# Optimization experiments

Hardware: AMD Instinct MI355X
Metric: run time of the kernel (lower is better)

Reference implementation:

```python
import jax, jax.numpy as jnp
import numpy as np

HEADS = 8
DIM_HEAD = 64
SCALE = DIM_HEAD ** -0.5


def setup_inputs() -> dict:
    key = jax.random.key(0)
    k1, k2, k3 = jax.random.split(key, 3)
    b, n, dim = 2, 4096, 512
    inner = HEADS * DIM_HEAD
    x = jax.random.normal(k1, (b, n, dim), dtype=jnp.float32)
    w_qkv = jax.random.normal(k2, (dim, 3 * inner), dtype=jnp.float32) * (dim ** -0.5)
    w_out = jax.random.normal(k3, (inner, dim), dtype=jnp.float32) * (inner ** -0.5)
    b_out = jnp.zeros((dim,), dtype=jnp.float32)
    return {"x": x, "w_qkv": w_qkv, "w_out": w_out, "b_out": b_out}


def reference(x, w_qkv, w_out, b_out):
    b, n, dim = x.shape
    qkv = x @ w_qkv  # [b, n, 3*inner]
    q, k, v = jnp.split(qkv, 3, axis=-1)
    # b n (h d) -> b h n d
    split_heads = lambda t: t.reshape(b, n, HEADS, DIM_HEAD).transpose(0, 2, 1, 3)
    q, k, v = split_heads(q), split_heads(k), split_heads(v)
    dots = jnp.einsum('bhid,bhjd->bhij', q, k) * SCALE  # [b, h, n, n]
    attn = jax.nn.log_softmax(dots, axis=-1)  # NOTE: log-softmax, not softmax
    out = jnp.einsum('bhij,bhjd->bhid', attn, v)  # [b, h, n, d]
    out = out.transpose(0, 2, 1, 3).reshape(b, n, HEADS * DIM_HEAD)
    return out @ w_out + b_out + x
```

## Files before the change

kernel.cpp:

```cpp
#include <hip/hip_runtime.h>
#include <stdint.h>

#define NSEQ   4096
#define BATCH  2
#define NHEAD  8
#define DHEAD  64
#define DIM    512
#define NQKV   1536
#define MROWS  (BATCH*NSEQ)
#define NBH    (BATCH*NHEAD)

typedef float  f32x4 __attribute__((ext_vector_type(4)));
typedef short  s16x8 __attribute__((ext_vector_type(8)));

__device__ __forceinline__ unsigned short f2b(float f){
  unsigned int u = __float_as_uint(f);
  u += 0x7FFFu + ((u >> 16) & 1u);
  return (unsigned short)(u >> 16);
}
__device__ __forceinline__ float b2f(unsigned short h){
  return __uint_as_float(((unsigned int)h) << 16);
}
__device__ __forceinline__ void gld_lds16(const void* g, void* l){
  __builtin_amdgcn_global_load_lds((const __attribute__((address_space(1))) unsigned int*)g,
                                   (__attribute__((address_space(3))) unsigned int*)l, 16, 0, 0);
}

__global__ void k_cvt(const float* __restrict__ in, unsigned short* __restrict__ out, int n4){
  int i = blockIdx.x*blockDim.x + threadIdx.x;
  if (i < n4){
    float4 v = ((const float4*)in)[i];
    ushort4 o;
    o.x = f2b(v.x); o.y = f2b(v.y); o.z = f2b(v.z); o.w = f2b(v.w);
    ((ushort4*)out)[i] = o;
  }
}

__global__ void k_transpose(const float* __restrict__ in, unsigned short* __restrict__ out, int R, int C){
  __shared__ float t[32][33];
  const int cb = blockIdx.x*32, rb = blockIdx.y*32;
  const int tx = threadIdx.x & 31, ty = threadIdx.x >> 5;
  #pragma unroll
  for (int s = 0; s < 32; s += 8) t[ty+s][tx] = in[(size_t)(rb+ty+s)*C + cb + tx];
  __syncthreads();
  #pragma unroll
  for (int s = 0; s < 32; s += 8) out[(size_t)(cb+ty+s)*R + rb + tx] = f2b(t[tx][ty+s]);
}

__global__ __launch_bounds__(256) void k_qkv_gemm(
    const unsigned short* __restrict__ A,
    const unsigned short* __restrict__ Bt,
    unsigned short* __restrict__ qbuf, unsigned short* __restrict__ kbuf,
    unsigned short* __restrict__ vbuf){
  __shared__ __align__(16) unsigned short at[128*32];
  __shared__ __align__(16) unsigned short bt[128*32];
  const int n0 = blockIdx.x*128, m0 = blockIdx.y*128;
  const int tid = threadIdx.x, w = tid>>6, lane = tid&63;
  const int wr = (w>>1)*64, wc = (w&1)*64;
  f32x4 acc[4][4] = {};
  for (int ks = 0; ks < 16; ++ks){
    const int k0 = ks*32;
    #pragma unroll
    for (int i = 0; i < 2; ++i){
      const int slot = w*2 + i;
      const int r = slot*16 + (lane>>2);
      const int ch = (lane&3) ^ (r&3);
      gld_lds16(A  + (size_t)(m0+r)*DIM + k0 + ch*8, (char*)at + slot*1024);
      gld_lds16(Bt + (size_t)(n0+r)*DIM + k0 + ch*8, (char*)bt + slot*1024);
    }
    __syncthreads();
    s16x8 af[4], bfr[4];
    #pragma unroll
    for (int f = 0; f < 4; ++f){
      const int rr = wr + f*16 + (lane&15);
      af[f]  = *(const s16x8*)((const char*)at + rr*64 + ((((lane>>4)) ^ (rr&3))<<4));
      const int cc = wc + f*16 + (lane&15);
      bfr[f] = *(const s16x8*)((const char*)bt + cc*64 + ((((lane>>4)) ^ (cc&3))<<4));
    }
    #pragma unroll
    for (int fr = 0; fr < 4; ++fr)
      #pragma unroll
      for (int fc = 0; fc < 4; ++fc)
        acc[fr][fc] = __builtin_amdgcn_mfma_f32_16x16x32_bf16(af[fr], bfr[fc], acc[fr][fc], 0,0,0);
    __syncthreads();
  }
  const float QS = 0.18033688011112042f;
  #pragma unroll
  for (int fr = 0; fr < 4; ++fr){
    #pragma unroll
    for (int fc = 0; fc < 4; ++fc){
      const int col = n0 + wc + fc*16 + (lane&15);
      const int which = col >> 9;
      const int h = (col & 511) >> 6;
      const int d = col & 63;
      unsigned short* dst = (which==0) ? qbuf : ((which==1) ? kbuf : vbuf);
      #pragma unroll
      for (int r = 0; r < 4; ++r){
        const int row = m0 + wr + fr*16 + (lane>>4)*4 + r;
        const int b = row >> 12, n = row & 4095;
        float v = acc[fr][fc][r];
        if (which == 0) v *= QS;
        dst[(size_t)((b*NHEAD + h)*NSEQ + n)*DHEAD + d] = f2b(v);
      }
    }
  }
}

__global__ __launch_bounds__(256) void k_tpart(
    const unsigned short* __restrict__ kbuf, const unsigned short* __restrict__ vbuf,
    float* __restrict__ tpart, float* __restrict__ vsp){
  __shared__ __align__(16) unsigned short kt[64*64];
  __shared__ __align__(16) unsigned short vt[64*64];
  const int bh = blockIdx.y, jc = blockIdx.x;
  const unsigned short* K = kbuf + (size_t)bh*NSEQ*DHEAD;
  const unsigned short* V = vbuf + (size_t)bh*NSEQ*DHEAD;
  const int tid = threadIdx.x;
  const int d1 = (tid>>4)<<2, d2 = (tid&15)<<2;
  const int j0 = jc*64;
  #pragma unroll
  for (int c = 0; c < 2; ++c){
    const int q = tid + 256*c;
    const int row = q>>3, ch = q&7;
    *(float4*)((char*)kt + row*128 + ch*16) = *(const float4*)((const char*)K + (size_t)(j0+row)*128 + ch*16);
    *(float4*)((char*)vt + row*128 + ch*16) = *(const float4*)((const char*)V + (size_t)(j0+row)*128 + ch*16);
  }
  __syncthreads();
  float accT[4][4] = {{0.f}};
  float accV[4] = {0.f,0.f,0.f,0.f};
  for (int jj = 0; jj < 64; ++jj){
    const ushort4 k4 = *(const ushort4*)(kt + jj*64 + d1);
    const ushort4 v4 = *(const ushort4*)(vt + jj*64 + d2);
    float kf[4] = {b2f(k4.x), b2f(k4.y), b2f(k4.z), b2f(k4.w)};
    float vf[4] = {b2f(v4.x), b2f(v4.y), b2f(v4.z), b2f(v4.w)};
    #pragma unroll
    for (int a = 0; a < 4; ++a)
      #pragma unroll
      for (int b = 0; b < 4; ++b) accT[a][b] += kf[a]*vf[b];
    #pragma unroll
    for (int b = 0; b < 4; ++b) accV[b] += vf[b];
  }
  float* tp = tpart + ((size_t)bh*64 + jc)*4096;
  #pragma unroll
  for (int a = 0; a < 4; ++a)
    #pragma unroll
    for (int b = 0; b < 4; ++b) tp[(d1+a)*64 + (d2+b)] = accT[a][b];
  if (tid < 16){
    #pragma unroll
    for (int b = 0; b < 4; ++b) vsp[((size_t)bh*64 + jc)*64 + d2 + b] = accV[b];
  }
}

__global__ void k_tred(const float* __restrict__ tpart, const float* __restrict__ vsp,
                       unsigned short* __restrict__ TB, float* __restrict__ vsum){
  const int blk = blockIdx.x;
  const int bh = blk >> 4, part = blk & 15;
  const int tid = threadIdx.x;
  const int idx = part*256 + tid;
  const int dd1 = idx>>6, dd2 = idx&63;
  float s = 0.f;
  #pragma unroll 8
  for (int pr = 0; pr < 64; ++pr) s += tpart[((size_t)bh*64 + pr)*4096 + idx];
  TB[(size_t)bh*4096 + dd2*64 + dd1] = f2b(s);
  if (part == 0 && tid < 64){
    float v = 0.f;
    #pragma unroll 8
    for (int pr = 0; pr < 64; ++pr) v += vsp[((size_t)bh*64 + pr)*64 + tid];
    vsum[bh*64 + tid] = v;
  }
}

#define KSTAGE(TT, DST) do { \
    const size_t joff_ = (size_t)(TT)*64*DHEAD; \
    gld_lds16(kg0 + joff_, (char*)(DST) + s0*1024); \
    gld_lds16(kg1 + joff_, (char*)(DST) + s1*1024); } while(0)

#define KTILE(BUF) do { \
    const char* buf_ = (const char*)(BUF); \
    _Pragma("unroll") \
    for (int kk = 0; kk < 4; ++kk){ \
      const int r_ = kk*16 + (lane&15); \
      const s16x8 b0_ = *(const s16x8*)(buf_ + r_*128 + ((((lane>>4))  ^ (r_&7))<<4)); \
      const s16x8 b1_ = *(const s16x8*)(buf_ + r_*128 + (((4+(lane>>4)) ^ (r_&7))<<4)); \
      f32x4 acc_ = {0.f,0.f,0.f,0.f}; \
      acc_ = __builtin_amdgcn_mfma_f32_16x16x32_bf16(aq0, b0_, acc_, 0,0,0); \
      acc_ = __builtin_amdgcn_mfma_f32_16x16x32_bf16(aq1, b1_, acc_, 0,0,0); \
      _Pragma("unroll") \
      for (int rr = 0; rr < 4; ++rr) lsum[rr] += __builtin_amdgcn_exp2f(acc_[rr]); \
    } } while(0)

__global__ __launch_bounds__(256) void k_attn(
    const unsigned short* __restrict__ qbuf, const unsigned short* __restrict__ kbuf,
    const unsigned short* __restrict__ TB, const float* __restrict__ vsum,
    unsigned short* __restrict__ om){
  __shared__ __align__(16) unsigned short kt[2][64*64];
  const int bid = blockIdx.x;
  const int idx = bid >> 3;
  const int bh = ((bid & 7) << 1) + (idx >> 6);
  const int qchunk = idx & 63;
  const int tid = threadIdx.x, w = tid>>6, lane = tid&63;
  const int q0 = qchunk*64 + w*16;
  const unsigned short* Q = qbuf + (size_t)bh*NSEQ*DHEAD;
  const unsigned short* K = kbuf + (size_t)bh*NSEQ*DHEAD;

  const int qrow = q0 + (lane&15);
  const s16x8 aq0 = *(const s16x8*)(Q + (size_t)qrow*DHEAD + ((lane>>4)<<3));
  const s16x8 aq1 = *(const s16x8*)(Q + (size_t)qrow*DHEAD + 32 + ((lane>>4)<<3));

  const int s0 = w*2, s1 = w*2 + 1;
  const int srow0 = s0*8 + (lane>>3), srow1 = s1*8 + (lane>>3);
  const int sch = ((lane&7) ^ (lane>>3));
  const unsigned short* kg0 = K + (size_t)srow0*DHEAD + sch*8;
  const unsigned short* kg1 = K + (size_t)srow1*DHEAD + sch*8;

  KSTAGE(0, kt[0]);
  __syncthreads();

  float lsum[4] = {0.f,0.f,0.f,0.f};
  for (int t = 0; t < 64; t += 2){
    KSTAGE(t+1, kt[1]);
    KTILE(kt[0]);
    __syncthreads();
    if (t + 2 < 64) KSTAGE(t+2, kt[0]);
    KTILE(kt[1]);
    __syncthreads();
  }

  #pragma unroll
  for (int m = 1; m < 16; m <<= 1)
    #pragma unroll
    for (int r = 0; r < 4; ++r) lsum[r] += __shfl_xor(lsum[r], m, 16);
  float lse2[4];
  #pragma unroll
  for (int r = 0; r < 4; ++r) lse2[r] = log2f(lsum[r]);

  const unsigned short* tb = TB + (size_t)bh*4096;
  const int b = bh>>3, h = bh&7;
  #pragma unroll
  for (int fc = 0; fc < 4; ++fc){
    const int d2 = fc*16 + (lane&15);
    const s16x8 t0 = *(const s16x8*)(tb + d2*64 + ((lane>>4)<<3));
    const s16x8 t1 = *(const s16x8*)(tb + d2*64 + 32 + ((lane>>4)<<3));
    const float vs = vsum[bh*64 + d2];
    f32x4 acc = {0.f,0.f,0.f,0.f};
    acc = __builtin_amdgcn_mfma_f32_16x16x32_bf16(aq0, t0, acc, 0,0,0);
    acc = __builtin_amdgcn_mfma_f32_16x16x32_bf16(aq1, t1, acc, 0,0,0);
    #pragma unroll
    for (int r = 0; r < 4; ++r){
      const int n = q0 + (lane>>4)*4 + r;
      const float val = 0.6931471805599453f * (acc[r] - lse2[r]*vs);
      om[((size_t)b*NSEQ + n)*DIM + h*DHEAD + d2] = f2b(val);
    }
  }
}

__global__ __launch_bounds__(256) void k_out_gemm(
    const unsigned short* __restrict__ A,
    const unsigned short* __restrict__ Bt,
    const float* __restrict__ bias, const float* __restrict__ xres,
    float* __restrict__ out){
  __shared__ __align__(16) unsigned short at[128*32];
  __shared__ __align__(16) unsigned short bt[128*32];
  const int n0 = blockIdx.x*128, m0 = blockIdx.y*128;
  const int tid = threadIdx.x, w = tid>>6, lane = tid&63;
  const int wr = (w>>1)*64, wc = (w&1)*64;
  f32x4 acc[4][4] = {};
  for (int ks = 0; ks < 16; ++ks){
    const int k0 = ks*32;
    #pragma unroll
    for (int i = 0; i < 2; ++i){
      const int slot = w*2 + i;
      const int r = slot*16 + (lane>>2);
      const int ch = (lane&3) ^ (r&3);
      gld_lds16(A  + (size_t)(m0+r)*DIM + k0 + ch*8, (char*)at + slot*1024);
      gld_lds16(Bt + (size_t)(n0+r)*DIM + k0 + ch*8, (char*)bt + slot*1024);
    }
    __syncthreads();
    s16x8 af[4], bfr[4];
    #pragma unroll
    for (int f = 0; f < 4; ++f){
      const int rr = wr + f*16 + (lane&15);
      af[f]  = *(const s16x8*)((const char*)at + rr*64 + ((((lane>>4)) ^ (rr&3))<<4));
      const int cc = wc + f*16 + (lane&15);
      bfr[f] = *(const s16x8*)((const char*)bt + cc*64 + ((((lane>>4)) ^ (cc&3))<<4));
    }
    #pragma unroll
    for (int fr = 0; fr < 4; ++fr)
      #pragma unroll
      for (int fc = 0; fc < 4; ++fc)
        acc[fr][fc] = __builtin_amdgcn_mfma_f32_16x16x32_bf16(af[fr], bfr[fc], acc[fr][fc], 0,0,0);
    __syncthreads();
  }
  #pragma unroll
  for (int fr = 0; fr < 4; ++fr){
    #pragma unroll
    for (int fc = 0; fc < 4; ++fc){
      const int col = n0 + wc + fc*16 + (lane&15);
      const float bb = bias[col];
      #pragma unroll
      for (int r = 0; r < 4; ++r){
        const int row = m0 + wr + fr*16 + (lane>>4)*4 + r;
        out[(size_t)row*DIM + col] = acc[fr][fc][r] + bb + xres[(size_t)row*DIM + col];
      }
    }
  }
}

extern "C" void kernel_launch(void* const* d_in, const int* in_sizes, int n_in,
                              void* d_out, int out_size, void* d_ws, size_t ws_size,
                              hipStream_t stream){
  const float* x    = (const float*)d_in[0];
  const float* wqkv = (const float*)d_in[1];
  const float* wout = (const float*)d_in[2];
  const float* bout = (const float*)d_in[3];
  float* out = (float*)d_out;

  char* p = (char*)d_ws;
  unsigned short* xb   = (unsigned short*)p; p += (size_t)MROWS*DIM*2;
  unsigned short* wqT  = (unsigned short*)p; p += (size_t)NQKV*DIM*2;
  unsigned short* woT  = (unsigned short*)p; p += (size_t)DIM*DIM*2;
  unsigned short* qbuf = (unsigned short*)p; p += (size_t)NBH*NSEQ*DHEAD*2;
  unsigned short* kbuf = (unsigned short*)p; p += (size_t)NBH*NSEQ*DHEAD*2;
  unsigned short* vbuf = (unsigned short*)p; p += (size_t)NBH*NSEQ*DHEAD*2;
  float* tpart         = (float*)p;          p += (size_t)NBH*64*64*64*4;
  float* vsp           = (float*)p;          p += (size_t)NBH*64*64*4;
  unsigned short* TB   = (unsigned short*)p; p += (size_t)NBH*64*64*2;
  float* vsum          = (float*)p;          p += (size_t)NBH*64*4;
  unsigned short* om   = (unsigned short*)p; p += (size_t)MROWS*DIM*2;

  k_cvt<<<dim3((MROWS*DIM/4 + 255)/256), dim3(256), 0, stream>>>(x, xb, MROWS*DIM/4);
  k_transpose<<<dim3(NQKV/32, DIM/32), dim3(256), 0, stream>>>(wqkv, wqT, DIM, NQKV);
  k_transpose<<<dim3(DIM/32, DIM/32), dim3(256), 0, stream>>>(wout, woT, DIM, DIM);
  k_qkv_gemm<<<dim3(NQKV/128, MROWS/128), dim3(256), 0, stream>>>(xb, wqT, qbuf, kbuf, vbuf);
  k_tpart<<<dim3(64, NBH), dim3(256), 0, stream>>>(kbuf, vbuf, tpart, vsp);
  k_tred<<<dim3(256), dim3(256), 0, stream>>>(tpart, vsp, TB, vsum);
  k_attn<<<dim3(1024), dim3(256), 0, stream>>>(qbuf, kbuf, TB, vsum, om);
  k_out_gemm<<<dim3(DIM/128, MROWS/128), dim3(256), 0, stream>>>(om, woT, bout, x, out);
}
```

Before: 132.3 us.

## Split attention logsumexp over key halves with 4-stage K pipeline and finalize kernel

The log-sum-exp pass now has each wave handle 32 query rows, two MFMA groups sharing every K fragment, and the key range is split in two halves across blocks. K tiles stream through a 4-deep LDS ring with explicit vmcnt waits and raw barriers, start at a staggered tile offset per block, and raise wave priority around the MFMAs. Partial sums go to a new workspace buffer and a separate finalize kernel combines them, takes the log and applies the Q·T projection. This roughly halves K LDS reads per MFMA and improves latency hiding, at the cost of an extra launch and extra global traffic for the partial sums.

```diff
diff --git a/kernel.cpp b/kernel.cpp
--- a/kernel.cpp
+++ b/kernel.cpp
@@ -169,42 +169,28 @@
   }
 }
 
-#define KSTAGE(TT, DST) do { \
-    const size_t joff_ = (size_t)(TT)*64*DHEAD; \
-    gld_lds16(kg0 + joff_, (char*)(DST) + s0*1024); \
-    gld_lds16(kg1 + joff_, (char*)(DST) + s1*1024); } while(0)
-
-#define KTILE(BUF) do { \
-    const char* buf_ = (const char*)(BUF); \
-    _Pragma("unroll") \
-    for (int kk = 0; kk < 4; ++kk){ \
-      const int r_ = kk*16 + (lane&15); \
-      const s16x8 b0_ = *(const s16x8*)(buf_ + r_*128 + ((((lane>>4))  ^ (r_&7))<<4)); \
-      const s16x8 b1_ = *(const s16x8*)(buf_ + r_*128 + (((4+(lane>>4)) ^ (r_&7))<<4)); \
-      f32x4 acc_ = {0.f,0.f,0.f,0.f}; \
-      acc_ = __builtin_amdgcn_mfma_f32_16x16x32_bf16(aq0, b0_, acc_, 0,0,0); \
-      acc_ = __builtin_amdgcn_mfma_f32_16x16x32_bf16(aq1, b1_, acc_, 0,0,0); \
-      _Pragma("unroll") \
-      for (int rr = 0; rr < 4; ++rr) lsum[rr] += __builtin_amdgcn_exp2f(acc_[rr]); \
-    } } while(0)
-
 __global__ __launch_bounds__(256) void k_attn(
     const unsigned short* __restrict__ qbuf, const unsigned short* __restrict__ kbuf,
-    const unsigned short* __restrict__ TB, const float* __restrict__ vsum,
-    unsigned short* __restrict__ om){
-  __shared__ __align__(16) unsigned short kt[2][64*64];
+    float* __restrict__ ps){
+  __shared__ __align__(16) unsigned short kt[4][64*64];
   const int bid = blockIdx.x;
   const int idx = bid >> 3;
-  const int bh = ((bid & 7) << 1) + (idx >> 6);
-  const int qchunk = idx & 63;
+  const int bh  = ((bid & 7) << 1) + (idx >> 6);
+  const int rest = idx & 63;
+  const int qchunk = rest >> 1;
+  const int jh = rest & 1;
   const int tid = threadIdx.x, w = tid>>6, lane = tid&63;
-  const int q0 = qchunk*64 + w*16;
+  const int q0 = qchunk*128 + w*32;
   const unsigned short* Q = qbuf + (size_t)bh*NSEQ*DHEAD;
   const unsigned short* K = kbuf + (size_t)bh*NSEQ*DHEAD;
 
-  const int qrow = q0 + (lane&15);
-  const s16x8 aq0 = *(const s16x8*)(Q + (size_t)qrow*DHEAD + ((lane>>4)<<3));
-  const s16x8 aq1 = *(const s16x8*)(Q + (size_t)qrow*DHEAD + 32 + ((lane>>4)<<3));
+  s16x8 aq[2][2];
+  #pragma unroll
+  for (int g = 0; g < 2; ++g){
+    const int qrow = q0 + g*16 + (lane&15);
+    aq[g][0] = *(const s16x8*)(Q + (size_t)qrow*DHEAD + ((lane>>4)<<3));
+    aq[g][1] = *(const s16x8*)(Q + (size_t)qrow*DHEAD + 32 + ((lane>>4)<<3));
+  }
 
   const int s0 = w*2, s1 = w*2 + 1;
   const int srow0 = s0*8 + (lane>>3), srow1 = s1*8 + (lane>>3);
@@ -212,27 +198,89 @@
   const unsigned short* kg0 = K + (size_t)srow0*DHEAD + sch*8;
   const unsigned short* kg1 = K + (size_t)srow1*DHEAD + sch*8;
 
-  KSTAGE(0, kt[0]);
-  __syncthreads();
-
-  float lsum[4] = {0.f,0.f,0.f,0.f};
-  for (int t = 0; t < 64; t += 2){
-    KSTAGE(t+1, kt[1]);
-    KTILE(kt[0]);
-    __syncthreads();
-    if (t + 2 < 64) KSTAGE(t+2, kt[0]);
-    KTILE(kt[1]);
-    __syncthreads();
+  const int phase = (idx*7) & 31;
+  const int jbase = jh*32;
+
+  {
+    const size_t o0 = (size_t)(jbase + ((0+phase)&31))*64*DHEAD;
+    gld_lds16(kg0 + o0, (char*)kt[0] + s0*1024);
+    gld_lds16(kg1 + o0, (char*)kt[0] + s1*1024);
+    const size_t o1 = (size_t)(jbase + ((1+phase)&31))*64*DHEAD;
+    gld_lds16(kg0 + o1, (char*)kt[1] + s0*1024);
+    gld_lds16(kg1 + o1, (char*)kt[1] + s1*1024);
+  }
+
+  float lsum[2][4] = {};
+  #pragma unroll
+  for (int u = 0; u < 32; ++u){
+    if (u < 31) { asm volatile("s_waitcnt vmcnt(2)" ::: "memory"); }
+    else        { asm volatile("s_waitcnt vmcnt(0)" ::: "memory"); }
+    __builtin_amdgcn_s_barrier();
+    asm volatile("" ::: "memory");
+    if (u < 30){
+      const size_t o = (size_t)(jbase + ((u+2+phase)&31))*64*DHEAD;
+      char* d = (char*)kt[(u+2)&3];
+      gld_lds16(kg0 + o, d + s0*1024);
+      gld_lds16(kg1 + o, d + s1*1024);
+    }
+    const char* buf = (const char*)kt[u&3];
+    #pragma unroll
+    for (int kk = 0; kk < 4; ++kk){
+      const int r = kk*16 + (lane&15);
+      const s16x8 b0 = *(const s16x8*)(buf + r*128 + ((((lane>>4))   ^ (r&7))<<4));
+      const s16x8 b1 = *(const s16x8*)(buf + r*128 + (((4+(lane>>4)) ^ (r&7))<<4));
+      __builtin_amdgcn_s_setprio(1);
+      f32x4 a0 = {0.f,0.f,0.f,0.f}, a1 = {0.f,0.f,0.f,0.f};
+      a0 = __builtin_amdgcn_mfma_f32_16x16x32_bf16(aq[0][0], b0, a0, 0,0,0);
+      a0 = __builtin_amdgcn_mfma_f32_16x16x32_bf16(aq[0][1], b1, a0, 0,0,0);
+      a1 = __builtin_amdgcn_mfma_f32_16x16x32_bf16(aq[1][0], b0, a1, 0,0,0);
+      a1 = __builtin_amdgcn_mfma_f32_16x16x32_bf16(aq[1][1], b1, a1, 0,0,0);
+      __builtin_amdgcn_s_setprio(0);
+      #pragma unroll
+      for (int rr = 0; rr < 4; ++rr){
+        lsum[0][rr] += __builtin_amdgcn_exp2f(a0[rr]);
+        lsum[1][rr] += __builtin_amdgcn_exp2f(a1[rr]);
+      }
+    }
   }
 
   #pragma unroll
   for (int m = 1; m < 16; m <<= 1)
     #pragma unroll
-    for (int r = 0; r < 4; ++r) lsum[r] += __shfl_xor(lsum[r], m, 16);
+    for (int g = 0; g < 2; ++g)
+      #pragma unroll
+      for (int r = 0; r < 4; ++r) lsum[g][r] += __shfl_xor(lsum[g][r], m, 16);
+
+  if ((lane&15) == 0){
+    float* pp = ps + ((size_t)jh*NBH + bh)*NSEQ;
+    #pragma unroll
+    for (int g = 0; g < 2; ++g)
+      #pragma unroll
+      for (int r = 0; r < 4; ++r)
+        pp[q0 + g*16 + (lane>>4)*4 + r] = lsum[g][r];
+  }
+}
+
+__global__ __launch_bounds__(256) void k_attn_fin(
+    const unsigned short* __restrict__ qbuf, const unsigned short* __restrict__ TB,
+    const float* __restrict__ vsum, const float* __restrict__ ps,
+    unsigned short* __restrict__ om){
+  const int bid = blockIdx.x;
+  const int bh = bid >> 6, qchunk = bid & 63;
+  const int tid = threadIdx.x, w = tid>>6, lane = tid&63;
+  const int q0 = qchunk*64 + w*16;
+  const unsigned short* Q = qbuf + (size_t)bh*NSEQ*DHEAD;
+  const int qrow = q0 + (lane&15);
+  const s16x8 aq0 = *(const s16x8*)(Q + (size_t)qrow*DHEAD + ((lane>>4)<<3));
+  const s16x8 aq1 = *(const s16x8*)(Q + (size_t)qrow*DHEAD + 32 + ((lane>>4)<<3));
+  const float* p0 = ps + (size_t)bh*NSEQ;
+  const float* p1 = ps + ((size_t)NBH + bh)*NSEQ;
   float lse2[4];
   #pragma unroll
-  for (int r = 0; r < 4; ++r) lse2[r] = log2f(lsum[r]);
-
+  for (int r = 0; r < 4; ++r){
+    const int n = q0 + (lane>>4)*4 + r;
+    lse2[r] = log2f(p0[n] + p1[n]);
+  }
   const unsigned short* tb = TB + (size_t)bh*4096;
   const int b = bh>>3, h = bh&7;
   #pragma unroll
@@ -326,6 +374,7 @@
   unsigned short* TB   = (unsigned short*)p; p += (size_t)NBH*64*64*2;
   float* vsum          = (float*)p;          p += (size_t)NBH*64*4;
   unsigned short* om   = (unsigned short*)p; p += (size_t)MROWS*DIM*2;
+  float* ps            = (float*)p;          p += (size_t)2*NBH*NSEQ*4;
 
   k_cvt<<<dim3((MROWS*DIM/4 + 255)/256), dim3(256), 0, stream>>>(x, xb, MROWS*DIM/4);
   k_transpose<<<dim3(NQKV/32, DIM/32), dim3(256), 0, stream>>>(wqkv, wqT, DIM, NQKV);
@@ -333,6 +382,7 @@
   k_qkv_gemm<<<dim3(NQKV/128, MROWS/128), dim3(256), 0, stream>>>(xb, wqT, qbuf, kbuf, vbuf);
   k_tpart<<<dim3(64, NBH), dim3(256), 0, stream>>>(kbuf, vbuf, tpart, vsp);
   k_tred<<<dim3(256), dim3(256), 0, stream>>>(tpart, vsp, TB, vsum);
-  k_attn<<<dim3(1024), dim3(256), 0, stream>>>(qbuf, kbuf, TB, vsum, om);
+  k_attn<<<dim3(1024), dim3(256), 0, stream>>>(qbuf, kbuf, ps);
+  k_attn_fin<<<dim3(1024), dim3(256), 0, stream>>>(qbuf, TB, vsum, ps, om);
   k_out_gemm<<<dim3(DIM/128, MROWS/128), dim3(256), 0, stream>>>(om, woT, bout, x, out);
 }
```

Result: faster. 128.2 us (-3.1%).

## Split attention logsumexp over key chunks with more queries per wave and deeper staging

Applied to the files above, without the earlier changes.

The attention kernel now gives each wave 64 query rows instead of 16, so every K tile loaded into LDS is reused four times. Each block handles one quarter of the key range. Partial exp-sums go to a workspace, and a new finishing kernel combines them to compute the output projection term. K staging uses a 4-buffer ring with explicit vmcnt waits, raw barriers and setprio around the MFMAs. Separately, the per-chunk T partials are stored as bf16 instead of fp32 to cut reduction traffic, at some cost in accuracy and one extra launch.

```diff
diff --git a/kernel.cpp b/kernel.cpp
--- a/kernel.cpp
+++ b/kernel.cpp
@@ -108,7 +108,7 @@
 
 __global__ __launch_bounds__(256) void k_tpart(
     const unsigned short* __restrict__ kbuf, const unsigned short* __restrict__ vbuf,
-    float* __restrict__ tpart, float* __restrict__ vsp){
+    unsigned short* __restrict__ tpart, float* __restrict__ vsp){
   __shared__ __align__(16) unsigned short kt[64*64];
   __shared__ __align__(16) unsigned short vt[64*64];
   const int bh = blockIdx.y, jc = blockIdx.x;
@@ -139,18 +139,18 @@
     #pragma unroll
     for (int b = 0; b < 4; ++b) accV[b] += vf[b];
   }
-  float* tp = tpart + ((size_t)bh*64 + jc)*4096;
+  unsigned short* tp = tpart + ((size_t)bh*64 + jc)*4096;
   #pragma unroll
   for (int a = 0; a < 4; ++a)
     #pragma unroll
-    for (int b = 0; b < 4; ++b) tp[(d1+a)*64 + (d2+b)] = accT[a][b];
+    for (int b = 0; b < 4; ++b) tp[(d1+a)*64 + (d2+b)] = f2b(accT[a][b]);
   if (tid < 16){
     #pragma unroll
     for (int b = 0; b < 4; ++b) vsp[((size_t)bh*64 + jc)*64 + d2 + b] = accV[b];
   }
 }
 
-__global__ void k_tred(const float* __restrict__ tpart, const float* __restrict__ vsp,
+__global__ void k_tred(const unsigned short* __restrict__ tpart, const float* __restrict__ vsp,
                        unsigned short* __restrict__ TB, float* __restrict__ vsum){
   const int blk = blockIdx.x;
   const int bh = blk >> 4, part = blk & 15;
@@ -159,7 +159,7 @@
   const int dd1 = idx>>6, dd2 = idx&63;
   float s = 0.f;
   #pragma unroll 8
-  for (int pr = 0; pr < 64; ++pr) s += tpart[((size_t)bh*64 + pr)*4096 + idx];
+  for (int pr = 0; pr < 64; ++pr) s += b2f(tpart[((size_t)bh*64 + pr)*4096 + idx]);
   TB[(size_t)bh*4096 + dd2*64 + dd1] = f2b(s);
   if (part == 0 && tid < 64){
     float v = 0.f;
@@ -169,42 +169,71 @@
   }
 }
 
-#define KSTAGE(TT, DST) do { \
-    const size_t joff_ = (size_t)(TT)*64*DHEAD; \
-    gld_lds16(kg0 + joff_, (char*)(DST) + s0*1024); \
-    gld_lds16(kg1 + joff_, (char*)(DST) + s1*1024); } while(0)
-
-#define KTILE(BUF) do { \
+#define ASTAGE(U, BUFI) do { \
+    const int ti_ = jbase + (((U)+phase)&15); \
+    const size_t o_ = (size_t)ti_*64*DHEAD; \
+    char* d_ = (char*)kt[BUFI]; \
+    gld_lds16(kg0 + o_, d_ + s0*1024); \
+    gld_lds16(kg1 + o_, d_ + s1*1024); } while(0)
+
+#define ATILE(BUF) do { \
     const char* buf_ = (const char*)(BUF); \
     _Pragma("unroll") \
     for (int kk = 0; kk < 4; ++kk){ \
       const int r_ = kk*16 + (lane&15); \
-      const s16x8 b0_ = *(const s16x8*)(buf_ + r_*128 + ((((lane>>4))  ^ (r_&7))<<4)); \
+      const s16x8 b0_ = *(const s16x8*)(buf_ + r_*128 + ((((lane>>4))   ^ (r_&7))<<4)); \
       const s16x8 b1_ = *(const s16x8*)(buf_ + r_*128 + (((4+(lane>>4)) ^ (r_&7))<<4)); \
-      f32x4 acc_ = {0.f,0.f,0.f,0.f}; \
-      acc_ = __builtin_amdgcn_mfma_f32_16x16x32_bf16(aq0, b0_, acc_, 0,0,0); \
-      acc_ = __builtin_amdgcn_mfma_f32_16x16x32_bf16(aq1, b1_, acc_, 0,0,0); \
+      f32x4 a0_ = {0.f,0.f,0.f,0.f}, a1_ = {0.f,0.f,0.f,0.f}; \
+      f32x4 a2_ = {0.f,0.f,0.f,0.f}, a3_ = {0.f,0.f,0.f,0.f}; \
+      __builtin_amdgcn_s_setprio(1); \
+      a0_ = __builtin_amdgcn_mfma_f32_16x16x32_bf16(aq[0][0], b0_, a0_, 0,0,0); \
+      a0_ = __builtin_amdgcn_mfma_f32_16x16x32_bf16(aq[0][1], b1_, a0_, 0,0,0); \
+      a1_ = __builtin_amdgcn_mfma_f32_16x16x32_bf16(aq[1][0], b0_, a1_, 0,0,0); \
+      a1_ = __builtin_amdgcn_mfma_f32_16x16x32_bf16(aq[1][1], b1_, a1_, 0,0,0); \
+      a2_ = __builtin_amdgcn_mfma_f32_16x16x32_bf16(aq[2][0], b0_, a2_, 0,0,0); \
+      a2_ = __builtin_amdgcn_mfma_f32_16x16x32_bf16(aq[2][1], b1_, a2_, 0,0,0); \
+      a3_ = __builtin_amdgcn_mfma_f32_16x16x32_bf16(aq[3][0], b0_, a3_, 0,0,0); \
+      a3_ = __builtin_amdgcn_mfma_f32_16x16x32_bf16(aq[3][1], b1_, a3_, 0,0,0); \
+      __builtin_amdgcn_s_setprio(0); \
       _Pragma("unroll") \
-      for (int rr = 0; rr < 4; ++rr) lsum[rr] += __builtin_amdgcn_exp2f(acc_[rr]); \
+      for (int rr = 0; rr < 4; ++rr){ \
+        lsum[0][rr] += __builtin_amdgcn_exp2f(a0_[rr]); \
+        lsum[1][rr] += __builtin_amdgcn_exp2f(a1_[rr]); \
+        lsum[2][rr] += __builtin_amdgcn_exp2f(a2_[rr]); \
+        lsum[3][rr] += __builtin_amdgcn_exp2f(a3_[rr]); \
+      } \
     } } while(0)
 
-__global__ __launch_bounds__(256) void k_attn(
+#define APHASE(U, LASTW) do { \
+    if (LASTW) { asm volatile("s_waitcnt vmcnt(0)" ::: "memory"); } \
+    else       { asm volatile("s_waitcnt vmcnt(2)" ::: "memory"); } \
+    __builtin_amdgcn_s_barrier(); \
+    asm volatile("" ::: "memory"); \
+    if ((U) < 14) ASTAGE((U)+2, ((U)+2)&3); \
+    ATILE(kt[(U)&3]); } while(0)
+
+__global__ __launch_bounds__(256, 4) void k_attn(
     const unsigned short* __restrict__ qbuf, const unsigned short* __restrict__ kbuf,
-    const unsigned short* __restrict__ TB, const float* __restrict__ vsum,
-    unsigned short* __restrict__ om){
-  __shared__ __align__(16) unsigned short kt[2][64*64];
+    float* __restrict__ ps){
+  __shared__ __align__(16) unsigned short kt[4][64*64];
   const int bid = blockIdx.x;
   const int idx = bid >> 3;
-  const int bh = ((bid & 7) << 1) + (idx >> 6);
-  const int qchunk = idx & 63;
+  const int bh  = ((bid & 7) << 1) + (idx >> 6);
+  const int rest = idx & 63;
+  const int qchunk = rest >> 2;
+  const int js = rest & 3;
   const int tid = threadIdx.x, w = tid>>6, lane = tid&63;
-  const int q0 = qchunk*64 + w*16;
+  const int q0 = qchunk*256 + w*64;
   const unsigned short* Q = qbuf + (size_t)bh*NSEQ*DHEAD;
   const unsigned short* K = kbuf + (size_t)bh*NSEQ*DHEAD;
 
-  const int qrow = q0 + (lane&15);
-  const s16x8 aq0 = *(const s16x8*)(Q + (size_t)qrow*DHEAD + ((lane>>4)<<3));
-  const s16x8 aq1 = *(const s16x8*)(Q + (size_t)qrow*DHEAD + 32 + ((lane>>4)<<3));
+  s16x8 aq[4][2];
+  #pragma unroll
+  for (int g = 0; g < 4; ++g){
+    const int qrow = q0 + g*16 + (lane&15);
+    aq[g][0] = *(const s16x8*)(Q + (size_t)qrow*DHEAD + ((lane>>4)<<3));
+    aq[g][1] = *(const s16x8*)(Q + (size_t)qrow*DHEAD + 32 + ((lane>>4)<<3));
+  }
 
   const int s0 = w*2, s1 = w*2 + 1;
   const int srow0 = s0*8 + (lane>>3), srow1 = s1*8 + (lane>>3);
@@ -212,27 +241,57 @@
   const unsigned short* kg0 = K + (size_t)srow0*DHEAD + sch*8;
   const unsigned short* kg1 = K + (size_t)srow1*DHEAD + sch*8;
 
-  KSTAGE(0, kt[0]);
-  __syncthreads();
-
-  float lsum[4] = {0.f,0.f,0.f,0.f};
-  for (int t = 0; t < 64; t += 2){
-    KSTAGE(t+1, kt[1]);
-    KTILE(kt[0]);
-    __syncthreads();
-    if (t + 2 < 64) KSTAGE(t+2, kt[0]);
-    KTILE(kt[1]);
-    __syncthreads();
-  }
+  const int phase = (idx*5) & 15;
+  const int jbase = js*16;
+
+  ASTAGE(0, 0);
+  ASTAGE(1, 1);
+
+  float lsum[4][4] = {};
+  APHASE(0,false);  APHASE(1,false);  APHASE(2,false);  APHASE(3,false);
+  APHASE(4,false);  APHASE(5,false);  APHASE(6,false);  APHASE(7,false);
+  APHASE(8,false);  APHASE(9,false);  APHASE(10,false); APHASE(11,false);
+  APHASE(12,false); APHASE(13,false); APHASE(14,false); APHASE(15,true);
 
   #pragma unroll
   for (int m = 1; m < 16; m <<= 1)
     #pragma unroll
-    for (int r = 0; r < 4; ++r) lsum[r] += __shfl_xor(lsum[r], m, 16);
+    for (int g = 0; g < 4; ++g)
+      #pragma unroll
+      for (int r = 0; r < 4; ++r) lsum[g][r] += __shfl_xor(lsum[g][r], m, 16);
+
+  if ((lane&15) == 0){
+    float* pp = ps + ((size_t)js*NBH + bh)*NSEQ;
+    #pragma unroll
+    for (int g = 0; g < 4; ++g)
+      #pragma unroll
+      for (int r = 0; r < 4; ++r)
+        pp[q0 + g*16 + (lane>>4)*4 + r] = lsum[g][r];
+  }
+}
+
+__global__ __launch_bounds__(256) void k_attn_fin(
+    const unsigned short* __restrict__ qbuf, const unsigned short* __restrict__ TB,
+    const float* __restrict__ vsum, const float* __restrict__ ps,
+    unsigned short* __restrict__ om){
+  const int bid = blockIdx.x;
+  const int bh = bid >> 6, qchunk = bid & 63;
+  const int tid = threadIdx.x, w = tid>>6, lane = tid&63;
+  const int q0 = qchunk*64 + w*16;
+  const unsigned short* Q = qbuf + (size_t)bh*NSEQ*DHEAD;
+  const int qrow = q0 + (lane&15);
+  const s16x8 aq0 = *(const s16x8*)(Q + (size_t)qrow*DHEAD + ((lane>>4)<<3));
+  const s16x8 aq1 = *(const s16x8*)(Q + (size_t)qrow*DHEAD + 32 + ((lane>>4)<<3));
+  const float* p0 = ps + (size_t)bh*NSEQ;
+  const float* p1 = ps + ((size_t)NBH   + bh)*NSEQ;
+  const float* p2 = ps + ((size_t)2*NBH + bh)*NSEQ;
+  const float* p3 = ps + ((size_t)3*NBH + bh)*NSEQ;
   float lse2[4];
   #pragma unroll
-  for (int r = 0; r < 4; ++r) lse2[r] = log2f(lsum[r]);
-
+  for (int r = 0; r < 4; ++r){
+    const int n = q0 + (lane>>4)*4 + r;
+    lse2[r] = log2f((p0[n] + p1[n]) + (p2[n] + p3[n]));
+  }
   const unsigned short* tb = TB + (size_t)bh*4096;
   const int b = bh>>3, h = bh&7;
   #pragma unroll
@@ -321,11 +380,12 @@
   unsigned short* qbuf = (unsigned short*)p; p += (size_t)NBH*NSEQ*DHEAD*2;
   unsigned short* kbuf = (unsigned short*)p; p += (size_t)NBH*NSEQ*DHEAD*2;
   unsigned short* vbuf = (unsigned short*)p; p += (size_t)NBH*NSEQ*DHEAD*2;
-  float* tpart         = (float*)p;          p += (size_t)NBH*64*64*64*4;
+  unsigned short* tpart= (unsigned short*)p; p += (size_t)NBH*64*4096*2;
   float* vsp           = (float*)p;          p += (size_t)NBH*64*64*4;
   unsigned short* TB   = (unsigned short*)p; p += (size_t)NBH*64*64*2;
   float* vsum          = (float*)p;          p += (size_t)NBH*64*4;
   unsigned short* om   = (unsigned short*)p; p += (size_t)MROWS*DIM*2;
+  float* ps            = (float*)p;          p += (size_t)4*NBH*NSEQ*4;
 
   k_cvt<<<dim3((MROWS*DIM/4 + 255)/256), dim3(256), 0, stream>>>(x, xb, MROWS*DIM/4);
   k_transpose<<<dim3(NQKV/32, DIM/32), dim3(256), 0, stream>>>(wqkv, wqT, DIM, NQKV);
@@ -333,6 +393,7 @@
   k_qkv_gemm<<<dim3(NQKV/128, MROWS/128), dim3(256), 0, stream>>>(xb, wqT, qbuf, kbuf, vbuf);
   k_tpart<<<dim3(64, NBH), dim3(256), 0, stream>>>(kbuf, vbuf, tpart, vsp);
   k_tred<<<dim3(256), dim3(256), 0, stream>>>(tpart, vsp, TB, vsum);
-  k_attn<<<dim3(1024), dim3(256), 0, stream>>>(qbuf, kbuf, TB, vsum, om);
+  k_attn<<<dim3(1024), dim3(256), 0, stream>>>(qbuf, kbuf, ps);
+  k_attn_fin<<<dim3(1024), dim3(256), 0, stream>>>(qbuf, TB, vsum, ps, om);
   k_out_gemm<<<dim3(DIM/128, MROWS/128), dim3(256), 0, stream>>>(om, woT, bout, x, out);
 }
```

Measured after the change: 211.2 us. 59.6% more time.
